# Performance work log

Hardware: AMD Instinct MI355X
Metric: run time of the kernel (lower is better)

The kernel has to match this reference:

```python
import jax, jax.numpy as jnp
import numpy as np

N_NODES = 50000
N_DIRECTED = 800000  # symmetrized to 1.6M (src,dst) pairs
IN_FEAT = 256
HEADS = 8
OUT = 64


def setup_inputs() -> dict:
    key = jax.random.key(0)
    k1, k2, k3, k4, k5 = jax.random.split(key, 5)
    r = jax.random.randint(k1, (N_DIRECTED,), 0, N_NODES)
    c = jax.random.randint(k2, (N_DIRECTED,), 0, N_NODES)
    # symmetric adjacency (values = 1), as edge list
    src = jnp.concatenate([r, c])
    dst = jnp.concatenate([c, r])
    x = jax.random.normal(k3, (N_NODES, IN_FEAT), dtype=jnp.float32)
    Ws = jax.random.normal(k4, (HEADS, OUT, IN_FEAT), dtype=jnp.float32) * 0.05
    As = jax.random.normal(k5, (HEADS, 2 * OUT, 1), dtype=jnp.float32) * 0.05
    return {"x": x, "src": src, "dst": dst, "Ws": Ws, "As": As}


def reference(x, src, dst, Ws, As):
    H, O, F = Ws.shape
    N = x.shape[0]
    # t_nodes = inputs @ Ws^T  -> [H, N, O]
    t = jnp.einsum('nf,hof->hno', x, Ws)
    a_l = As[:, :O, 0]   # [H, O]
    a_r = As[:, O:, 0]   # [H, O]
    Al = jnp.einsum('hno,ho->hn', t, a_l)  # [H, N]
    Ar = jnp.einsum('hno,ho->hn', t, a_r)  # [H, N]
    outs = []
    for k in range(H):
        # sparse E[i,j] = Al[i] + Ar[j] on adjacency pattern
        e = Al[k][src] + Ar[k][dst]  # [E]
        # NOTE: original applies tf.sparse.softmax to E directly (its lrelu
        # tensor is computed but never used), so no leaky_relu here.
        m = jax.ops.segment_max(e, src, num_segments=N)
        ex = jnp.exp(e - m[src])
        den = jax.ops.segment_sum(ex, src, num_segments=N)
        alpha = ex / den[src]
        # sparse_dense_matmul(alphas, t_nodes[k])
        h = jax.ops.segment_sum(alpha[:, None] * t[k][dst], src, num_segments=N)
        outs.append(h)
    out = jnp.stack(outs, axis=1)          # [N, H, O]
    out = out.reshape(N, H * O)            # reduction=False -> concat heads
    return jax.nn.elu(out)
```

## Files before the change

### kernel.cpp

```cpp
#include <hip/hip_runtime.h>
#include <hip/hip_bf16.h>

#define NN 50000
#define INF 256
#define NH 8
#define OUTF 64
#define NC 512
#define NTILES 782
#define EPB 8192
#define NBK 391
#define NBX 12501

typedef __attribute__((ext_vector_type(8))) short bf16x8;
typedef __attribute__((ext_vector_type(4))) float f32x4;
typedef __attribute__((ext_vector_type(2))) float v2f;
typedef __attribute__((ext_vector_type(8))) float f32x8;
typedef unsigned long long u64;

__device__ __forceinline__ unsigned short f2bf(float f){
  unsigned u = __float_as_uint(f);
  u += 0x7FFFu + ((u>>16)&1u);
  return (unsigned short)(u>>16);
}

#define GLOAD_LDS16(g, s) \
  __builtin_amdgcn_global_load_lds((const __attribute__((address_space(1))) void*)(g), \
                                   (__attribute__((address_space(3))) void*)(s), 16, 0, 0)

__global__ __launch_bounds__(256) void k_prep_w(const float* __restrict__ W,
                                                unsigned short* __restrict__ Wt){
  const int tid = threadIdx.x;
  const int r = tid>>2, cb = (tid&3)*64;
  char* tile = (char*)(Wt + (size_t)blockIdx.x*16384);
  const float* Wr = W + ((long)blockIdx.x*64 + r)*INF;
#pragma unroll
  for (int i=0;i<16;i++){
    int c = cb + i*4;
    float4 v = *(const float4*)(Wr + c);
    ushort4 b; b.x=f2bf(v.x); b.y=f2bf(v.y); b.z=f2bf(v.z); b.w=f2bf(v.w);
    int addr = r*512 + ((((c>>3) ^ (r&7)))<<4) + ((c&7)<<1);
    *(ushort4*)(tile + addr) = b;
  }
}

__global__ void k_atil(const float* __restrict__ W, const float* __restrict__ As,
                       float* __restrict__ atil){
  const int h = blockIdx.x, f = threadIdx.x;
  float s = 0.f;
  for (int o=0;o<64;o++) s += W[((long)h*64+o)*INF + f] * As[h*128 + 64 + o];
  atil[h*256 + f] = s;
}

__global__ __launch_bounds__(256) void k_xbar_bhist(const float* __restrict__ x,
                                                    const float* __restrict__ atil,
                                                    unsigned short* __restrict__ xb,
                                                    float* __restrict__ eAr,
                                                    const int* __restrict__ src,
                                                    int* __restrict__ M,
                                                    int E, int NB){
  __shared__ int hh[NBK];
  const int tid = threadIdx.x;
  if (blockIdx.x >= NBX){
    const int b = blockIdx.x - NBX;
    for (int i=tid;i<NBK;i+=256) hh[i]=0;
    __syncthreads();
    const int base = b*EPB;
    const int lim = min(E-base, EPB);
    for (int i=tid;i<lim;i+=256) atomicAdd(&hh[src[base+i]>>7], 1);
    __syncthreads();
    for (int i=tid;i<NBK;i+=256) M[(long)i*NB + b] = hh[i];
    return;
  }
  const int w = tid>>6, l = tid&63;
  const long n = (long)blockIdx.x*4 + w;
  if (n > NN) return;
  if (n == NN){
    uint2 z; z.x=0; z.y=0;
    *(uint2*)((char*)xb + (size_t)n*512 + l*8) = z;
    if (l < 8) eAr[n*NH + l] = 0.f;
    return;
  }
  float4 v = *(const float4*)(x + n*INF + l*4);
  uint2 d;
  d.x = (unsigned)f2bf(v.x) | ((unsigned)f2bf(v.y)<<16);
  d.y = (unsigned)f2bf(v.z) | ((unsigned)f2bf(v.w)<<16);
  *(uint2*)((char*)xb + (size_t)n*512 + l*8) = d;
  float p[8];
#pragma unroll
  for (int h=0;h<8;h++){
    float4 a = *(const float4*)(atil + h*256 + l*4);
    p[h] = v.x*a.x + v.y*a.y + v.z*a.z + v.w*a.w;
  }
#pragma unroll
  for (int off=1; off<64; off<<=1){
#pragma unroll
    for (int h=0;h<8;h++) p[h] += __shfl_xor(p[h], off, 64);
  }
  if (l < 8){
    float e = p[0];
#pragma unroll
    for (int h=1;h<8;h++) if (l==h) e = p[h];
    eAr[n*NH + l] = __expf(e);
  }
}

__global__ __launch_bounds__(256) void k_bscan(int* __restrict__ M,
                                               int* __restrict__ tot, int NB){
  __shared__ int lds[256];
  const int k = blockIdx.x, tid = threadIdx.x;
  int v = (tid<NB) ? M[(long)k*NB+tid] : 0;
  const int orig = v;
  lds[tid]=v; __syncthreads();
  for (int off=1; off<256; off<<=1){
    int a = (tid>=off)? lds[tid-off] : 0;
    __syncthreads(); lds[tid]+=a; __syncthreads();
  }
  if (tid<NB) M[(long)k*NB+tid] = lds[tid]-orig;
  if (tid==255) tot[k] = lds[255];
}

__global__ __launch_bounds__(512) void k_sscan(const int* __restrict__ in,
                                               int* __restrict__ out, int n){
  __shared__ int lds[512];
  const int tid = threadIdx.x;
  int v = (tid<n)? in[tid] : 0;
  const int orig = v;
  lds[tid]=v; __syncthreads();
  for (int off=1; off<512; off<<=1){
    int a = (tid>=off)? lds[tid-off] : 0;
    __syncthreads(); lds[tid]+=a; __syncthreads();
  }
  if (tid<=n) out[tid] = lds[tid]-orig;
}

__global__ __launch_bounds__(256) void k_bscat(const int* __restrict__ src,
                                               const int* __restrict__ dst,
                                               const int* __restrict__ M,
                                               const int* __restrict__ bOff,
                                               u64* __restrict__ ebuf,
                                               int E, int NB){
  __shared__ int cur[NBK];
  const int tid = threadIdx.x, b = blockIdx.x;
  for (int i=tid;i<NBK;i+=256) cur[i] = bOff[i] + M[(long)i*NB + b];
  __syncthreads();
  const int base = b*EPB;
  const int lim = min(E-base, EPB);
  for (int i=tid;i<lim;i+=256){
    int s = src[base+i], d = dst[base+i];
    int p = atomicAdd(&cur[s>>7], 1);
    ebuf[p] = ((u64)(unsigned)d<<32) | (unsigned)s;
  }
}

__global__ __launch_bounds__(256) void k_bcnt2(const u64* __restrict__ ebuf,
                                               const int* __restrict__ bOff,
                                               int* __restrict__ cnt,
                                               int* __restrict__ pbTot){
  __shared__ int h[128];
  __shared__ int ps[128];
  const int k = blockIdx.x, tid = threadIdx.x;
  if (tid<128) h[tid]=0;
  __syncthreads();
  const int beg = bOff[k], end = bOff[k+1];
  for (int i=beg+tid; i<end; i+=256)
    atomicAdd(&h[(int)(unsigned)ebuf[i] & 127], 1);
  __syncthreads();
  if (tid<128){
    cnt[(k<<7)+tid] = h[tid];
    ps[tid] = (h[tid]+7)&~7;
  }
  __syncthreads();
  for (int off=64; off>0; off>>=1){
    if (tid<off) ps[tid] += ps[tid+off];
    __syncthreads();
  }
  if (tid==0) pbTot[k] = ps[0];
}

__global__ __launch_bounds__(256) void k_final(const u64* __restrict__ ebuf,
                                               const int* __restrict__ bOff,
                                               const int* __restrict__ cnt,
                                               const int* __restrict__ pbOff,
                                               int* __restrict__ row_ptr,
                                               int* __restrict__ col){
  __shared__ int s[128];
  __shared__ int cur[128];
  __shared__ int pend[128];
  const int k = blockIdx.x, tid = threadIdx.x;
  int c = 0, pc = 0;
  if (tid<128){
    c = cnt[(k<<7)+tid];
    pc = (c+7)&~7;
    s[tid] = pc;
  }
  __syncthreads();
  for (int off=1; off<128; off<<=1){
    int a = (tid>=off && tid<128)? s[tid-off] : 0;
    __syncthreads();
    if (tid<128) s[tid] += a;
    __syncthreads();
  }
  const int base = pbOff[k];
  if (tid<128){
    int rp = base + s[tid] - pc;
    row_ptr[(k<<7)+tid] = rp;
    cur[tid] = rp;
    pend[tid] = rp + pc;
  }
  __syncthreads();
  const int beg = bOff[k], end = bOff[k+1];
  for (int i=beg+tid; i<end; i+=256){
    u64 e = ebuf[i];
    int sn = (int)(unsigned)e;
    int d  = (int)(e>>32);
    int p = atomicAdd(&cur[sn&127], 1);
    col[p] = d;
  }
  __syncthreads();
  if (tid<128){
    for (int i=cur[tid]; i<pend[tid]; i++) col[i] = NN;
  }
}

__global__ __launch_bounds__(256) void k_aggr2(const int* __restrict__ row_ptr,
                                               const int* __restrict__ col,
                                               const unsigned short* __restrict__ xb,
                                               const float* __restrict__ eAr,
                                               unsigned short* __restrict__ g,
                                               float* __restrict__ den,
                                               int tile0){
  const int tid = threadIdx.x, l = tid&63;
  const int wv = tid>>6;
  const int fh = blockIdx.x & 1;
  const long n = (long)tile0*64 + (blockIdx.x>>1)*4 + wv;
  if (n >= NN) return;
  const int beg = __builtin_amdgcn_readfirstlane(row_ptr[n]);
  const int end = __builtin_amdgcn_readfirstlane(row_ptr[n+1]);
  const char* xbp = (const char*)xb + fh*256;
  v2f acc[8] = {};
  float dnl = 0.f;
  const long l4 = (long)l*4;
  const int lw = l&7;

  for (int i=beg; i<end; i+=8){
    int cc[8];
#pragma unroll
    for (int e=0;e<8;e++) cc[e] = __builtin_amdgcn_readfirstlane(col[i+e]);
    unsigned q[8];
#pragma unroll
    for (int e=0;e<8;e++) q[e] = *(const unsigned*)(xbp + (size_t)cc[e]*512 + l4);
    float wl[8];
#pragma unroll
    for (int e=0;e<8;e++) wl[e] = eAr[(size_t)cc[e]*NH + lw];
#pragma unroll
    for (int e=0;e<8;e++) dnl += wl[e];
#pragma unroll
    for (int e=0;e<8;e++){
      f32x8 wv8 = *(const f32x8*)(eAr + (size_t)cc[e]*NH);
      v2f f01;
      f01.x = __uint_as_float(q[e]<<16);
      f01.y = __uint_as_float(q[e]&0xffff0000u);
#pragma unroll
      for (int h=0;h<8;h++){
        v2f w2; w2.x = wv8[h]; w2.y = wv8[h];
        acc[h] = __builtin_elementwise_fma(w2, f01, acc[h]);
      }
    }
  }

  const int lt = (int)(n>>6) - tile0;
  const int r  = (int)(n&63);
  const int f0 = fh*128 + l*2;
  char* tb = (char*)g + (size_t)lt*262144 + r*512
           + ((((f0>>3) ^ (r&7)))<<4) + ((f0&7)<<1);
#pragma unroll
  for (int h=0;h<8;h++){
    unsigned d = (unsigned)f2bf(acc[h].x) | ((unsigned)f2bf(acc[h].y)<<16);
    *(unsigned*)(tb + h*32768) = d;
  }
  if (fh==0 && l < 8) den[n*NH + l] = dnl;
}

__global__ __launch_bounds__(256) void k_gemm2(const unsigned short* __restrict__ g,
                                               const unsigned short* __restrict__ Wt,
                                               const float* __restrict__ den,
                                               float* __restrict__ out,
                                               int tile0){
  __shared__ unsigned short As[16384];
  __shared__ unsigned short Bs[16384];
  __shared__ float linv[64];
  const int tid = threadIdx.x, w = tid>>6, l = tid&63;
  const int brow = tile0 + blockIdx.x;
  const int h = blockIdx.y;
  {
    const char* srcA = (const char*)g + (size_t)blockIdx.x*262144 + h*32768 + w*8192 + l*16;
    char* dstA = (char*)As + w*8192;
#pragma unroll
    for (int k=0;k<8;k++) GLOAD_LDS16(srcA + k*1024, dstA + k*1024);
    const char* srcB = (const char*)Wt + (size_t)h*32768 + w*8192 + l*16;
    char* dstB = (char*)Bs + w*8192;
#pragma unroll
    for (int k=0;k<8;k++) GLOAD_LDS16(srcB + k*1024, dstB + k*1024);
  }
  if (tid < 64){
    long gr = (long)brow*64 + tid;
    float dv = (gr < NN) ? den[gr*NH + h] : 1.f;
    linv[tid] = dv > 0.f ? 1.f/dv : 0.f;
  }
  asm volatile("s_waitcnt vmcnt(0)");
  __syncthreads();

  const int col = w*16 + (l&15);
  f32x4 acc[4] = {};
#pragma unroll
  for (int ks=0; ks<8; ks++){
    int chunkB = (ks*4 + (l>>4)) ^ (col&7);
    bf16x8 bfrag = *(const bf16x8*)((char*)Bs + col*512 + (chunkB<<4));
#pragma unroll
    for (int mt=0; mt<4; mt++){
      int ar_ = mt*16 + (l&15);
      int chunkA = (ks*4 + (l>>4)) ^ (ar_&7);
      bf16x8 afrag = *(const bf16x8*)((char*)As + ar_*512 + (chunkA<<4));
      acc[mt] = __builtin_amdgcn_mfma_f32_16x16x32_bf16(afrag, bfrag, acc[mt], 0,0,0);
    }
  }
#pragma unroll
  for (int mt=0; mt<4; mt++){
#pragma unroll
    for (int j=0;j<4;j++){
      int r = mt*16 + (l>>4)*4 + j;
      long gr = (long)brow*64 + r;
      if (gr < NN){
        float v = acc[mt][j] * linv[r];
        out[gr*NC + h*64 + col] = v>0.f ? v : expm1f(v);
      }
    }
  }
}

extern "C" void kernel_launch(void* const* d_in, const int* in_sizes, int n_in,
                              void* d_out, int out_size, void* d_ws, size_t ws_size,
                              hipStream_t stream){
  const float* x   = (const float*)d_in[0];
  const int*   src = (const int*)d_in[1];
  const int*   dst = (const int*)d_in[2];
  const float* Ws  = (const float*)d_in[3];
  const float* Av  = (const float*)d_in[4];
  const int E = in_sizes[1];
  const int NB = (E + EPB - 1) / EPB;

  char* ws = (char*)d_ws;
  size_t off = 0;
  auto alloc = [&](size_t bytes)->void*{
    void* p = ws + off; off += (bytes + 255) & ~(size_t)255; return p;
  };
  unsigned short* xb   = (unsigned short*)alloc((size_t)50048*512);
  float* eAr           = (float*)alloc((size_t)50048*NH*4);
  float* atil          = (float*)alloc(8*256*4);
  float* den           = (float*)alloc((size_t)50048*NH*4);
  unsigned short* Wt   = (unsigned short*)alloc((size_t)8*32768);
  int*   cnt           = (int*)alloc(50304*4);
  int*   row_ptr       = (int*)alloc(50304*4);
  int*   M             = (int*)alloc((size_t)NBK*256*4);
  int*   tot           = (int*)alloc(512*4);
  int*   bOff          = (int*)alloc(512*4);
  int*   pbTot         = (int*)alloc(512*4);
  int*   pbOff         = (int*)alloc(512*4);
  int*   col           = (int*)alloc(((size_t)E + 8*50048 + 64)*4);

  size_t remain = (ws_size > off + 256) ? (ws_size - off - 256) : 0;
  int chunk = (int)(remain / 262144);
  if (chunk > NTILES) chunk = NTILES;
  if (chunk < 49) chunk = 49;
  unsigned short* g = (unsigned short*)alloc((size_t)chunk*262144);
  u64* ebuf = (u64*)g;

  k_prep_w<<<8,256,0,stream>>>(Ws, Wt);
  k_atil<<<8,256,0,stream>>>(Ws, Av, atil);
  k_xbar_bhist<<<NBX+NB,256,0,stream>>>(x, atil, xb, eAr, src, M, E, NB);

  k_bscan<<<NBK,256,0,stream>>>(M, tot, NB);
  k_sscan<<<1,512,0,stream>>>(tot, bOff, NBK);
  k_bscat<<<NB,256,0,stream>>>(src, dst, M, bOff, ebuf, E, NB);
  k_bcnt2<<<NBK,256,0,stream>>>(ebuf, bOff, cnt, pbTot);
  k_sscan<<<1,512,0,stream>>>(pbTot, pbOff, NBK);
  k_final<<<NBK,256,0,stream>>>(ebuf, bOff, cnt, pbOff, row_ptr, col);

  int tile0 = 0;
  while (tile0 < NTILES){
    int tiles = NTILES - tile0 < chunk ? NTILES - tile0 : chunk;
    k_aggr2<<<tiles*32,256,0,stream>>>(row_ptr, col, xb, eAr, g, den, tile0);
    k_gemm2<<<dim3(tiles,8),256,0,stream>>>(g, Wt, den, (float*)d_out, tile0);
    tile0 += tiles;
  }
}
```

Measured before the change: 333.1 us.

## Pack bucketed edges into 32-bit words, merge W prep into front kernel, remap aggregation waves

Edge records in the bucket scatter buffer are packed as dst<<7 | (src&127) in 32 bits instead of 64, which halves the traffic of the bucketing scatter and of the two passes that read it back. The separate W-to-bf16 prep kernel is folded into the combined front kernel, saving one launch, and the histogram blocks are placed ahead of the node-conversion blocks. In aggregation, the two feature halves of a node now run as two waves of the same block rather than in separate blocks, so each block covers 2 nodes. The minimum chunk size drops to 25 because the edge buffer is smaller.

```diff
diff --git a/kernel.cpp b/kernel.cpp
--- a/kernel.cpp
+++ b/kernel.cpp
@@ -15,7 +15,6 @@
 typedef __attribute__((ext_vector_type(4))) float f32x4;
 typedef __attribute__((ext_vector_type(2))) float v2f;
 typedef __attribute__((ext_vector_type(8))) float f32x8;
-typedef unsigned long long u64;
 
 __device__ __forceinline__ unsigned short f2bf(float f){
   unsigned u = __float_as_uint(f);
@@ -26,22 +25,6 @@
 #define GLOAD_LDS16(g, s) \
   __builtin_amdgcn_global_load_lds((const __attribute__((address_space(1))) void*)(g), \
                                    (__attribute__((address_space(3))) void*)(s), 16, 0, 0)
-
-__global__ __launch_bounds__(256) void k_prep_w(const float* __restrict__ W,
-                                                unsigned short* __restrict__ Wt){
-  const int tid = threadIdx.x;
-  const int r = tid>>2, cb = (tid&3)*64;
-  char* tile = (char*)(Wt + (size_t)blockIdx.x*16384);
-  const float* Wr = W + ((long)blockIdx.x*64 + r)*INF;
-#pragma unroll
-  for (int i=0;i<16;i++){
-    int c = cb + i*4;
-    float4 v = *(const float4*)(Wr + c);
-    ushort4 b; b.x=f2bf(v.x); b.y=f2bf(v.y); b.z=f2bf(v.z); b.w=f2bf(v.w);
-    int addr = r*512 + ((((c>>3) ^ (r&7)))<<4) + ((c&7)<<1);
-    *(ushort4*)(tile + addr) = b;
-  }
-}
 
 __global__ void k_atil(const float* __restrict__ W, const float* __restrict__ As,
                        float* __restrict__ atil){
@@ -51,17 +34,34 @@
   atil[h*256 + f] = s;
 }
 
-__global__ __launch_bounds__(256) void k_xbar_bhist(const float* __restrict__ x,
-                                                    const float* __restrict__ atil,
-                                                    unsigned short* __restrict__ xb,
-                                                    float* __restrict__ eAr,
-                                                    const int* __restrict__ src,
-                                                    int* __restrict__ M,
-                                                    int E, int NB){
+__global__ __launch_bounds__(256) void k_front(const float* __restrict__ x,
+                                               const float* __restrict__ W,
+                                               unsigned short* __restrict__ Wt,
+                                               const float* __restrict__ atil,
+                                               unsigned short* __restrict__ xb,
+                                               float* __restrict__ eAr,
+                                               const int* __restrict__ src,
+                                               int* __restrict__ M,
+                                               int E, int NB){
   __shared__ int hh[NBK];
   const int tid = threadIdx.x;
-  if (blockIdx.x >= NBX){
-    const int b = blockIdx.x - NBX;
+  const int bid = blockIdx.x;
+  if (bid < 8){
+    const int r = tid>>2, cb = (tid&3)*64;
+    char* tile = (char*)(Wt + (size_t)bid*16384);
+    const float* Wr = W + ((long)bid*64 + r)*INF;
+#pragma unroll
+    for (int i=0;i<16;i++){
+      int c = cb + i*4;
+      float4 v = *(const float4*)(Wr + c);
+      ushort4 b; b.x=f2bf(v.x); b.y=f2bf(v.y); b.z=f2bf(v.z); b.w=f2bf(v.w);
+      int addr = r*512 + ((((c>>3) ^ (r&7)))<<4) + ((c&7)<<1);
+      *(ushort4*)(tile + addr) = b;
+    }
+    return;
+  }
+  if (bid < 8+NB){
+    const int b = bid-8;
     for (int i=tid;i<NBK;i+=256) hh[i]=0;
     __syncthreads();
     const int base = b*EPB;
@@ -72,7 +72,7 @@
     return;
   }
   const int w = tid>>6, l = tid&63;
-  const long n = (long)blockIdx.x*4 + w;
+  const long n = (long)(bid-8-NB)*4 + w;
   if (n > NN) return;
   if (n == NN){
     uint2 z; z.x=0; z.y=0;
@@ -137,7 +137,7 @@
                                                const int* __restrict__ dst,
                                                const int* __restrict__ M,
                                                const int* __restrict__ bOff,
-                                               u64* __restrict__ ebuf,
+                                               unsigned* __restrict__ ebuf,
                                                int E, int NB){
   __shared__ int cur[NBK];
   const int tid = threadIdx.x, b = blockIdx.x;
@@ -148,11 +148,11 @@
   for (int i=tid;i<lim;i+=256){
     int s = src[base+i], d = dst[base+i];
     int p = atomicAdd(&cur[s>>7], 1);
-    ebuf[p] = ((u64)(unsigned)d<<32) | (unsigned)s;
-  }
-}
-
-__global__ __launch_bounds__(256) void k_bcnt2(const u64* __restrict__ ebuf,
+    ebuf[p] = ((unsigned)d<<7) | (unsigned)(s&127);
+  }
+}
+
+__global__ __launch_bounds__(256) void k_bcnt2(const unsigned* __restrict__ ebuf,
                                                const int* __restrict__ bOff,
                                                int* __restrict__ cnt,
                                                int* __restrict__ pbTot){
@@ -163,7 +163,7 @@
   __syncthreads();
   const int beg = bOff[k], end = bOff[k+1];
   for (int i=beg+tid; i<end; i+=256)
-    atomicAdd(&h[(int)(unsigned)ebuf[i] & 127], 1);
+    atomicAdd(&h[(int)(ebuf[i] & 127u)], 1);
   __syncthreads();
   if (tid<128){
     cnt[(k<<7)+tid] = h[tid];
@@ -177,7 +177,7 @@
   if (tid==0) pbTot[k] = ps[0];
 }
 
-__global__ __launch_bounds__(256) void k_final(const u64* __restrict__ ebuf,
+__global__ __launch_bounds__(256) void k_final(const unsigned* __restrict__ ebuf,
                                                const int* __restrict__ bOff,
                                                const int* __restrict__ cnt,
                                                const int* __restrict__ pbOff,
@@ -210,11 +210,9 @@
   __syncthreads();
   const int beg = bOff[k], end = bOff[k+1];
   for (int i=beg+tid; i<end; i+=256){
-    u64 e = ebuf[i];
-    int sn = (int)(unsigned)e;
-    int d  = (int)(e>>32);
-    int p = atomicAdd(&cur[sn&127], 1);
-    col[p] = d;
+    unsigned e = ebuf[i];
+    int p = atomicAdd(&cur[e & 127u], 1);
+    col[p] = (int)(e>>7);
   }
   __syncthreads();
   if (tid<128){
@@ -231,8 +229,8 @@
                                                int tile0){
   const int tid = threadIdx.x, l = tid&63;
   const int wv = tid>>6;
-  const int fh = blockIdx.x & 1;
-  const long n = (long)tile0*64 + (blockIdx.x>>1)*4 + wv;
+  const int fh = wv&1;
+  const long n = (long)tile0*64 + blockIdx.x*2 + (wv>>1);
   if (n >= NN) return;
   const int beg = __builtin_amdgcn_readfirstlane(row_ptr[n]);
   const int end = __builtin_amdgcn_readfirstlane(row_ptr[n+1]);
@@ -371,14 +369,12 @@
   size_t remain = (ws_size > off + 256) ? (ws_size - off - 256) : 0;
   int chunk = (int)(remain / 262144);
   if (chunk > NTILES) chunk = NTILES;
-  if (chunk < 49) chunk = 49;
+  if (chunk < 25) chunk = 25;
   unsigned short* g = (unsigned short*)alloc((size_t)chunk*262144);
-  u64* ebuf = (u64*)g;
-
-  k_prep_w<<<8,256,0,stream>>>(Ws, Wt);
+  unsigned* ebuf = (unsigned*)g;
+
   k_atil<<<8,256,0,stream>>>(Ws, Av, atil);
-  k_xbar_bhist<<<NBX+NB,256,0,stream>>>(x, atil, xb, eAr, src, M, E, NB);
-
+  k_front<<<8+NB+NBX,256,0,stream>>>(x, Ws, Wt, atil, xb, eAr, src, M, E, NB);
   k_bscan<<<NBK,256,0,stream>>>(M, tot, NB);
   k_sscan<<<1,512,0,stream>>>(tot, bOff, NBK);
   k_bscat<<<NB,256,0,stream>>>(src, dst, M, bOff, ebuf, E, NB);
```

Result: faster. 311.0 us (-6.6%).
